# Kernel optimization log

Measured on AMD Instinct MI355X. Metric: run time of the kernel, lower is better.

Reference implementation:

```python
import jax, jax.numpy as jnp
import numpy as np

EPS = 0.01                      # cfg.eps
INV_4PI = 1.0 / (4.0 * np.pi)   # 3D free-space Green's constant


def setup_inputs() -> dict:
    key = jax.random.key(0)
    k1, k2, k3 = jax.random.split(key, 3)
    B, M, d = 32768, 2048, 3
    return {
        "x_query": jax.random.normal(k1, (B, d), dtype=jnp.float32),
        "x_land": jax.random.normal(k2, (M, d), dtype=jnp.float32),
        "g_land": jax.random.normal(k3, (M,), dtype=jnp.float32),
    }


def reference(x_query, x_land, g_land):
    # Regularized 3D Poisson Green's function:
    #   G(x,y)      =  1/(4*pi) * (||x-y||^2 + eps^2)^(-1/2)
    #   grad_x G    = -1/(4*pi) * (x-y) * (||x-y||^2 + eps^2)^(-3/2)
    M = x_land.shape[0]
    r2 = (jnp.sum(x_query * x_query, axis=1)[:, None]
          - 2.0 * (x_query @ x_land.T)
          + jnp.sum(x_land * x_land, axis=1)[None, :])
    t = jnp.maximum(r2, 0.0) + EPS * EPS          # (B, M), regularized
    G = INV_4PI * jax.lax.rsqrt(t)                # (B, M)
    v_hat = (G * g_land[None, :]).sum(axis=1) / M # (B,)
    # fused gradient reduction: avoid materializing (B, M, d) dG.
    # sum_m g_m * dG = -1/(4pi) * [ x_q * sum_m c_m  -  c @ x_land ],
    # where c_m = g_m * t^(-3/2)
    c = g_land[None, :] * t ** (-1.5)             # (B, M)
    gradv_hat = -INV_4PI * (x_query * c.sum(axis=1, keepdims=True) - c @ x_land) / M
    return v_hat, gradv_hat
```

## Files before the change

kernel.cpp:

```cpp
#include <hip/hip_runtime.h>
#include <math.h>


#define EPS2      1e-4f
#define INV_4PI   0.07957747154594767f

constexpr int M_LAND = 2048;
constexpr int NW     = 16;
constexpr int SLICE  = M_LAND / NW;
constexpr int QPB    = 128;

__global__ __launch_bounds__(1024, 4)
void poisson_mc_kernel(const float* __restrict__ xq,
                       const float* __restrict__ xl,
                       const float* __restrict__ gl,
                       float* __restrict__ out,
                       int B)
{
    __shared__ float4 pack[M_LAND];
    __shared__ float4 gpack[M_LAND];
    __shared__ float  part[NW][QPB][5];

    const int tid = threadIdx.x;

    for (int j = tid; j < M_LAND; j += 1024) {
        float l0 = xl[3*j + 0];
        float l1 = xl[3*j + 1];
        float l2 = xl[3*j + 2];
        float g  = gl[j];
        float n2 = l0*l0 + l1*l1 + l2*l2 + EPS2;
        pack[j]  = make_float4(-2.0f*l0, -2.0f*l1, -2.0f*l2, n2);
        gpack[j] = make_float4(-2.0f*g*l0, -2.0f*g*l1, -2.0f*g*l2, g);
    }

    const int lane  = tid & 63;
    const int w     = tid >> 6;
    const int qbase = blockIdx.x * QPB;
    const int qa    = qbase + lane;
    const int qb    = qbase + 64 + lane;

    const float a0 = xq[3*qa+0], a1 = xq[3*qa+1], a2 = xq[3*qa+2];
    const float b0 = xq[3*qb+0], b1 = xq[3*qb+1], b2 = xq[3*qb+2];
    const float qea = a0*a0 + a1*a1 + a2*a2;
    const float qeb = b0*b0 + b1*b1 + b2*b2;

    __syncthreads();

    float av_a = 0.f, ac_a = 0.f, ax_a = 0.f, ay_a = 0.f, az_a = 0.f;
    float av_b = 0.f, ac_b = 0.f, ax_b = 0.f, ay_b = 0.f, az_b = 0.f;

    const int base = w * SLICE;
#pragma unroll 8
    for (int i = 0; i < SLICE; ++i) {
        const float4 p  = pack[base + i];
        const float4 gp = gpack[base + i];

        float ta = fmaf(p.x, a0, fmaf(p.y, a1, fmaf(p.z, a2, qea))) + p.w;
        ta = fmaxf(ta, EPS2);
        float sa  = __builtin_amdgcn_rsqf(ta);
        float s2a = sa * sa;
        float s3a = s2a * sa;
        av_a = fmaf(gp.w, sa,  av_a);
        ac_a = fmaf(gp.w, s3a, ac_a);
        ax_a = fmaf(s3a, gp.x, ax_a);
        ay_a = fmaf(s3a, gp.y, ay_a);
        az_a = fmaf(s3a, gp.z, az_a);

        float tb = fmaf(p.x, b0, fmaf(p.y, b1, fmaf(p.z, b2, qeb))) + p.w;
        tb = fmaxf(tb, EPS2);
        float sb  = __builtin_amdgcn_rsqf(tb);
        float s2b = sb * sb;
        float s3b = s2b * sb;
        av_b = fmaf(gp.w, sb,  av_b);
        ac_b = fmaf(gp.w, s3b, ac_b);
        ax_b = fmaf(s3b, gp.x, ax_b);
        ay_b = fmaf(s3b, gp.y, ay_b);
        az_b = fmaf(s3b, gp.z, az_b);
    }

    part[w][lane][0] = av_a;  part[w][lane][1] = ac_a;
    part[w][lane][2] = ax_a;  part[w][lane][3] = ay_a;  part[w][lane][4] = az_a;
    part[w][lane+64][0] = av_b;  part[w][lane+64][1] = ac_b;
    part[w][lane+64][2] = ax_b;  part[w][lane+64][3] = ay_b;  part[w][lane+64][4] = az_b;

    __syncthreads();

    if (tid < 512) {
        const int q   = tid >> 2;
        const int cmp = tid & 3;
        const int qg  = qbase + q;

        if (cmp == 0) {
            float s = 0.f;
            #pragma unroll
            for (int ww = 0; ww < NW; ++ww) s += part[ww][q][0];
            out[qg] = s * (INV_4PI / (float)M_LAND);
        } else {
            float sc = 0.f, sy = 0.f;
            #pragma unroll
            for (int ww = 0; ww < NW; ++ww) {
                sc += part[ww][q][1];
                sy += part[ww][q][1 + cmp];
            }
            const float qc = xq[3*qg + (cmp-1)];
            out[B + 3*qg + (cmp-1)] =
                (-INV_4PI / (float)M_LAND) * fmaf(qc, sc, 0.5f * sy);
        }
    }
}

extern "C" void kernel_launch(void* const* d_in, const int* in_sizes, int n_in,
                              void* d_out, int out_size, void* d_ws, size_t ws_size,
                              hipStream_t stream)
{
    const float* xq = (const float*)d_in[0];
    const float* xl = (const float*)d_in[1];
    const float* gl = (const float*)d_in[2];
    float* out = (float*)d_out;

    const int B = in_sizes[0] / 3;
    const int grid = B / QPB;

    poisson_mc_kernel<<<grid, 1024, 0, stream>>>(xq, xl, gl, out, B);
}
```

Baseline: 31.24 us.

## Pre-pack landmarks in workspace and stream them via scalar loads

Adds a small pre-pass kernel that writes the packed landmark data (8 floats per landmark) to the workspace once. The main kernel then reads each wave's wave-uniform slice through s_load_dwordx16 into scalar registers, double-buffered in inline asm, instead of building per-block LDS copies and reading them with LDS loads. This removes the per-block packing prologue, the LDS traffic and one barrier, and frees LDS. The costs are a second kernel launch, reliance on hand-written asm and explicit waitcnts, and a fallback to the old LDS kernel when the workspace is too small.

```diff
diff --git a/kernel.cpp b/kernel.cpp
--- a/kernel.cpp
+++ b/kernel.cpp
@@ -2,81 +2,103 @@
 #include <math.h>
 
 
-#define EPS2      1e-4f
-#define INV_4PI   0.07957747154594767f
+#define EPS2    1e-4f
+#define INV_4PI 0.07957747154594767f
 
 constexpr int M_LAND = 2048;
 constexpr int NW     = 16;
 constexpr int SLICE  = M_LAND / NW;
 constexpr int QPB    = 128;
+constexpr int NGRP   = SLICE / 2;
+
+typedef float f32x16 __attribute__((ext_vector_type(16)));
+
+__global__ void poisson_pack_kernel(const float* __restrict__ xl,
+                                    const float* __restrict__ gl,
+                                    float* __restrict__ ws)
+{
+    int j = blockIdx.x * 256 + threadIdx.x;
+    if (j < M_LAND) {
+        float l0 = xl[3*j], l1 = xl[3*j+1], l2 = xl[3*j+2], g = gl[j];
+        float n2 = l0*l0 + l1*l1 + l2*l2 + EPS2;
+        float* r = ws + 8*j;
+        r[0] = -2.0f*l0;   r[1] = -2.0f*l1;   r[2] = -2.0f*l2;   r[3] = n2;
+        r[4] = -2.0f*g*l0; r[5] = -2.0f*g*l1; r[6] = -2.0f*g*l2; r[7] = g;
+    }
+}
+
+#define LOAD1(D, P) \
+    asm volatile("s_load_dwordx16 %0, %1, 0x0" : "=&s"(D) : "s"(P))
+
+#define SWAIT() do { \
+    asm volatile("s_waitcnt lgkmcnt(0)" ::: "memory"); \
+    __builtin_amdgcn_sched_barrier(0); \
+} while (0)
+
+#define LM(PX,PY,PZ,PW,GX,GY,GZ,GG) do { \
+    float ta = fmaf((PX), a0, fmaf((PY), a1, fmaf((PZ), a2, qea))) + (PW); \
+    ta = fmaxf(ta, EPS2); \
+    float sa  = __builtin_amdgcn_rsqf(ta); \
+    float s3a = sa * sa * sa; \
+    av_a = fmaf((GG), sa,  av_a);  ac_a = fmaf((GG), s3a, ac_a); \
+    ax_a = fmaf(s3a, (GX), ax_a);  ay_a = fmaf(s3a, (GY), ay_a); \
+    az_a = fmaf(s3a, (GZ), az_a); \
+    float tb = fmaf((PX), b0, fmaf((PY), b1, fmaf((PZ), b2, qeb))) + (PW); \
+    tb = fmaxf(tb, EPS2); \
+    float sb  = __builtin_amdgcn_rsqf(tb); \
+    float s3b = sb * sb * sb; \
+    av_b = fmaf((GG), sb,  av_b);  ac_b = fmaf((GG), s3b, ac_b); \
+    ax_b = fmaf(s3b, (GX), ax_b);  ay_b = fmaf(s3b, (GY), ay_b); \
+    az_b = fmaf(s3b, (GZ), az_b); \
+} while (0)
+
+#define COMP2(D) do { \
+    LM(D[0],D[1],D[2],D[3],D[4],D[5],D[6],D[7]); \
+    LM(D[8],D[9],D[10],D[11],D[12],D[13],D[14],D[15]); \
+} while (0)
 
 __global__ __launch_bounds__(1024, 4)
-void poisson_mc_kernel(const float* __restrict__ xq,
-                       const float* __restrict__ xl,
-                       const float* __restrict__ gl,
-                       float* __restrict__ out,
-                       int B)
-{
-    __shared__ float4 pack[M_LAND];
-    __shared__ float4 gpack[M_LAND];
-    __shared__ float  part[NW][QPB][5];
-
-    const int tid = threadIdx.x;
-
-    for (int j = tid; j < M_LAND; j += 1024) {
-        float l0 = xl[3*j + 0];
-        float l1 = xl[3*j + 1];
-        float l2 = xl[3*j + 2];
-        float g  = gl[j];
-        float n2 = l0*l0 + l1*l1 + l2*l2 + EPS2;
-        pack[j]  = make_float4(-2.0f*l0, -2.0f*l1, -2.0f*l2, n2);
-        gpack[j] = make_float4(-2.0f*g*l0, -2.0f*g*l1, -2.0f*g*l2, g);
-    }
-
+void poisson_smem_kernel(const float* __restrict__ xq,
+                         const float* __restrict__ ws,
+                         float* __restrict__ out, int B)
+{
+    __shared__ float part[NW][QPB][5];
+
+    const int tid   = threadIdx.x;
     const int lane  = tid & 63;
     const int w     = tid >> 6;
     const int qbase = blockIdx.x * QPB;
     const int qa    = qbase + lane;
     const int qb    = qbase + 64 + lane;
 
-    const float a0 = xq[3*qa+0], a1 = xq[3*qa+1], a2 = xq[3*qa+2];
-    const float b0 = xq[3*qb+0], b1 = xq[3*qb+1], b2 = xq[3*qb+2];
+    const float a0 = xq[3*qa], a1 = xq[3*qa+1], a2 = xq[3*qa+2];
+    const float b0 = xq[3*qb], b1 = xq[3*qb+1], b2 = xq[3*qb+2];
     const float qea = a0*a0 + a1*a1 + a2*a2;
     const float qeb = b0*b0 + b1*b1 + b2*b2;
 
-    __syncthreads();
-
-    float av_a = 0.f, ac_a = 0.f, ax_a = 0.f, ay_a = 0.f, az_a = 0.f;
-    float av_b = 0.f, ac_b = 0.f, ax_b = 0.f, ay_b = 0.f, az_b = 0.f;
-
-    const int base = w * SLICE;
-#pragma unroll 8
-    for (int i = 0; i < SLICE; ++i) {
-        const float4 p  = pack[base + i];
-        const float4 gp = gpack[base + i];
-
-        float ta = fmaf(p.x, a0, fmaf(p.y, a1, fmaf(p.z, a2, qea))) + p.w;
-        ta = fmaxf(ta, EPS2);
-        float sa  = __builtin_amdgcn_rsqf(ta);
-        float s2a = sa * sa;
-        float s3a = s2a * sa;
-        av_a = fmaf(gp.w, sa,  av_a);
-        ac_a = fmaf(gp.w, s3a, ac_a);
-        ax_a = fmaf(s3a, gp.x, ax_a);
-        ay_a = fmaf(s3a, gp.y, ay_a);
-        az_a = fmaf(s3a, gp.z, az_a);
-
-        float tb = fmaf(p.x, b0, fmaf(p.y, b1, fmaf(p.z, b2, qeb))) + p.w;
-        tb = fmaxf(tb, EPS2);
-        float sb  = __builtin_amdgcn_rsqf(tb);
-        float s2b = sb * sb;
-        float s3b = s2b * sb;
-        av_b = fmaf(gp.w, sb,  av_b);
-        ac_b = fmaf(gp.w, s3b, ac_b);
-        ax_b = fmaf(s3b, gp.x, ax_b);
-        ay_b = fmaf(s3b, gp.y, ay_b);
-        az_b = fmaf(s3b, gp.z, az_b);
-    }
+    float av_a=0.f, ac_a=0.f, ax_a=0.f, ay_a=0.f, az_a=0.f;
+    float av_b=0.f, ac_b=0.f, ax_b=0.f, ay_b=0.f, az_b=0.f;
+
+    const int wu = __builtin_amdgcn_readfirstlane(w * SLICE);
+    const float* base = ws + (size_t)wu * 8;
+
+    f32x16 A, Bv;
+    LOAD1(A, base);
+    SWAIT();
+
+#pragma unroll 1
+    for (int g = 0; g + 2 < NGRP; g += 2) {
+        LOAD1(Bv, base + (g + 1) * 16);
+        COMP2(A);
+        SWAIT();
+        LOAD1(A, base + (g + 2) * 16);
+        COMP2(Bv);
+        SWAIT();
+    }
+    LOAD1(Bv, base + (NGRP - 1) * 16);
+    COMP2(A);
+    SWAIT();
+    COMP2(Bv);
 
     part[w][lane][0] = av_a;  part[w][lane][1] = ac_a;
     part[w][lane][2] = ax_a;  part[w][lane][3] = ay_a;  part[w][lane][4] = az_a;
@@ -89,7 +111,6 @@
         const int q   = tid >> 2;
         const int cmp = tid & 3;
         const int qg  = qbase + q;
-
         if (cmp == 0) {
             float s = 0.f;
             #pragma unroll
@@ -109,6 +130,80 @@
     }
 }
 
+__global__ __launch_bounds__(1024, 4)
+void poisson_lds_kernel(const float* __restrict__ xq,
+                        const float* __restrict__ xl,
+                        const float* __restrict__ gl,
+                        float* __restrict__ out, int B)
+{
+    __shared__ float4 pack[M_LAND];
+    __shared__ float4 gpack[M_LAND];
+    __shared__ float  part[NW][QPB][5];
+
+    const int tid = threadIdx.x;
+    for (int j = tid; j < M_LAND; j += 1024) {
+        float l0 = xl[3*j], l1 = xl[3*j+1], l2 = xl[3*j+2], g = gl[j];
+        float n2 = l0*l0 + l1*l1 + l2*l2 + EPS2;
+        pack[j]  = make_float4(-2.0f*l0, -2.0f*l1, -2.0f*l2, n2);
+        gpack[j] = make_float4(-2.0f*g*l0, -2.0f*g*l1, -2.0f*g*l2, g);
+    }
+    const int lane = tid & 63, w = tid >> 6;
+    const int qbase = blockIdx.x * QPB;
+    const int qa = qbase + lane, qb = qbase + 64 + lane;
+    const float a0 = xq[3*qa], a1 = xq[3*qa+1], a2 = xq[3*qa+2];
+    const float b0 = xq[3*qb], b1 = xq[3*qb+1], b2 = xq[3*qb+2];
+    const float qea = a0*a0 + a1*a1 + a2*a2;
+    const float qeb = b0*b0 + b1*b1 + b2*b2;
+    __syncthreads();
+
+    float av_a=0.f, ac_a=0.f, ax_a=0.f, ay_a=0.f, az_a=0.f;
+    float av_b=0.f, ac_b=0.f, ax_b=0.f, ay_b=0.f, az_b=0.f;
+    const int base = w * SLICE;
+#pragma unroll 8
+    for (int i = 0; i < SLICE; ++i) {
+        const float4 p  = pack[base + i];
+        const float4 gp = gpack[base + i];
+        float ta = fmaf(p.x, a0, fmaf(p.y, a1, fmaf(p.z, a2, qea))) + p.w;
+        ta = fmaxf(ta, EPS2);
+        float sa = __builtin_amdgcn_rsqf(ta);
+        float s3a = sa*sa*sa;
+        av_a = fmaf(gp.w, sa, av_a);  ac_a = fmaf(gp.w, s3a, ac_a);
+        ax_a = fmaf(s3a, gp.x, ax_a); ay_a = fmaf(s3a, gp.y, ay_a);
+        az_a = fmaf(s3a, gp.z, az_a);
+        float tb = fmaf(p.x, b0, fmaf(p.y, b1, fmaf(p.z, b2, qeb))) + p.w;
+        tb = fmaxf(tb, EPS2);
+        float sb = __builtin_amdgcn_rsqf(tb);
+        float s3b = sb*sb*sb;
+        av_b = fmaf(gp.w, sb, av_b);  ac_b = fmaf(gp.w, s3b, ac_b);
+        ax_b = fmaf(s3b, gp.x, ax_b); ay_b = fmaf(s3b, gp.y, ay_b);
+        az_b = fmaf(s3b, gp.z, az_b);
+    }
+    part[w][lane][0] = av_a;  part[w][lane][1] = ac_a;
+    part[w][lane][2] = ax_a;  part[w][lane][3] = ay_a;  part[w][lane][4] = az_a;
+    part[w][lane+64][0] = av_b;  part[w][lane+64][1] = ac_b;
+    part[w][lane+64][2] = ax_b;  part[w][lane+64][3] = ay_b;  part[w][lane+64][4] = az_b;
+    __syncthreads();
+    if (tid < 512) {
+        const int q = tid >> 2, cmp = tid & 3, qg = qbase + q;
+        if (cmp == 0) {
+            float s = 0.f;
+            #pragma unroll
+            for (int ww = 0; ww < NW; ++ww) s += part[ww][q][0];
+            out[qg] = s * (INV_4PI / (float)M_LAND);
+        } else {
+            float sc = 0.f, sy = 0.f;
+            #pragma unroll
+            for (int ww = 0; ww < NW; ++ww) {
+                sc += part[ww][q][1];
+                sy += part[ww][q][1 + cmp];
+            }
+            const float qc = xq[3*qg + (cmp-1)];
+            out[B + 3*qg + (cmp-1)] =
+                (-INV_4PI / (float)M_LAND) * fmaf(qc, sc, 0.5f * sy);
+        }
+    }
+}
+
 extern "C" void kernel_launch(void* const* d_in, const int* in_sizes, int n_in,
                               void* d_out, int out_size, void* d_ws, size_t ws_size,
                               hipStream_t stream)
@@ -118,8 +213,14 @@
     const float* gl = (const float*)d_in[2];
     float* out = (float*)d_out;
 
-    const int B = in_sizes[0] / 3;
+    const int B    = in_sizes[0] / 3;
     const int grid = B / QPB;
 
-    poisson_mc_kernel<<<grid, 1024, 0, stream>>>(xq, xl, gl, out, B);
-}
+    if (ws_size >= (size_t)(M_LAND * 8 * sizeof(float))) {
+        float* ws = (float*)d_ws;
+        poisson_pack_kernel<<<(M_LAND + 255) / 256, 256, 0, stream>>>(xl, gl, ws);
+        poisson_smem_kernel<<<grid, 1024, 0, stream>>>(xq, ws, out, B);
+    } else {
+        poisson_lds_kernel<<<grid, 1024, 0, stream>>>(xq, xl, gl, out, B);
+    }
+}
```

Result: slower. 41.98 us (+34.4%).
